# Kernel optimization log

Hardware: AMD Instinct MI355X
Metric: run time of the kernel (lower is better)

## Reference

```python
import jax, jax.numpy as jnp
import numpy as np

N_NODES = 10000
N_EDGES = 320000
HIDDEN = 256          # hidden_feat -> dim of gcn output x
MLP_IN = 2 * HIDDEN   # concat(src, dst)
OUT_FEATURES = 10


def setup_inputs() -> dict:
    key = jax.random.key(0)
    k_x, k_e, k_w1, k_w2 = jax.random.split(key, 4)
    x = jax.random.normal(k_x, (N_NODES, HIDDEN), dtype=jnp.float32)
    edge_index = jax.random.randint(k_e, (2, N_EDGES), 0, N_NODES, dtype=jnp.int64)
    # ClassifierMLP2(2*hidden_feat, out_features): Linear -> ReLU -> Linear -> log_softmax
    W1 = jax.random.normal(k_w1, (MLP_IN, HIDDEN), dtype=jnp.float32) * 0.02
    b1 = jnp.zeros((HIDDEN,), dtype=jnp.float32)
    W2 = jax.random.normal(k_w2, (HIDDEN, OUT_FEATURES), dtype=jnp.float32) * 0.02
    b2 = jnp.zeros((OUT_FEATURES,), dtype=jnp.float32)
    return {"x": x, "edge_index": edge_index, "W1": W1, "b1": b1, "W2": W2, "b2": b2}


def reference(x, edge_index, W1, b1, W2, b2):
    # mix_node_features(..., node_feat_mixing='cat'):
    # gather source/target node features per edge and concatenate -> [E, 2*H]
    src, dst = edge_index[0], edge_index[1]
    edges_x = jnp.concatenate([x[src], x[dst]], axis=1)  # [E, 2H]
    # ClassifierMLP2 forward
    h = jax.nn.relu(edges_x @ W1 + b1)                   # [E, H]
    logits = h @ W2 + b2                                 # [E, C]
    return jax.nn.log_softmax(logits, axis=-1)
```

## Files before the change

### kernel.cpp

```cpp
#include <hip/hip_runtime.h>

#define E_TOTAL 320000
#define NNODES  10000
#define HID     256
#define NCLS    10

typedef __attribute__((ext_vector_type(4))) float f32x4;
typedef __attribute__((ext_vector_type(2))) float f32x2;
typedef __attribute__((ext_vector_type(4))) unsigned int u32x4;
typedef __attribute__((ext_vector_type(8))) __bf16 bf16x8;
typedef __attribute__((ext_vector_type(8))) unsigned short u16x8;

static __device__ __forceinline__ unsigned short f2bf(float f) {
  unsigned u = __builtin_bit_cast(unsigned, f);
  u += 0x7fffu + ((u >> 16) & 1u);
  return (unsigned short)(u >> 16);
}

__global__ void k_pack(const float* __restrict__ x,
                       const float* __restrict__ W1,
                       const float* __restrict__ W2,
                       unsigned short* __restrict__ xbf,
                       unsigned short* __restrict__ w1f,
                       unsigned short* __restrict__ w2f) {
  int b = blockIdx.x, tid = threadIdx.x;
  if (b < 1250) {
    int i = b * 256 + tid;
    const f32x4* s = (const f32x4*)x + (size_t)i * 2;
    f32x4 a = s[0], c = s[1];
    u16x8 o;
    o[0]=f2bf(a[0]); o[1]=f2bf(a[1]); o[2]=f2bf(a[2]); o[3]=f2bf(a[3]);
    o[4]=f2bf(c[0]); o[5]=f2bf(c[1]); o[6]=f2bf(c[2]); o[7]=f2bf(c[3]);
    *((u16x8*)xbf + i) = o;
  } else if (b < 1314) {
    int gid = (b - 1250) * 256 + tid;
    int l = gid & 63, kk = (gid >> 6) & 7, cb = (gid >> 9) & 15, half = gid >> 13;
    int kbase = half * 256 + kk * 32 + (l >> 4) * 8;
    int col = cb * 16 + (l & 15);
    u16x8 o;
#pragma unroll
    for (int j = 0; j < 8; ++j) o[j] = f2bf(W1[(size_t)(kbase + j) * HID + col]);
    *((u16x8*)w1f + gid) = o;
  } else {
    int gid = (b - 1314) * 256 + tid;
    int l = gid & 63, kk = gid >> 6;
    int kbase = kk * 32 + (l >> 4) * 8;
    int c = l & 15;
    u16x8 o;
#pragma unroll
    for (int j = 0; j < 8; ++j)
      o[j] = (c < NCLS) ? f2bf(W2[(size_t)(kbase + j) * NCLS + c]) : (unsigned short)0;
    *((u16x8*)w2f + gid) = o;
  }
}

__global__ __launch_bounds__(256, 3) void k_prep(
    const unsigned short* __restrict__ xbf,
    const unsigned short* __restrict__ w1f,
    const float* __restrict__ b1,
    unsigned char* __restrict__ Yf8)
{
  __shared__ __align__(16) unsigned short ldsA[2][32 * 64];

  const int tid  = threadIdx.x;
  const int lane = tid & 63;
  const int wv   = tid >> 6;
  const int n0   = blockIdx.x * 32;
  const int half = blockIdx.y;
  const int l15  = lane & 15;
  const int lhi  = lane >> 4;

  f32x4 acc[2][4] = {};

  auto stageA = [&](int kb, int buf) {
    int col0 = kb * 64;
    int r = wv * 8 + (lane >> 3);
    int gr = n0 + r; if (gr > NNODES - 1) gr = NNODES - 1;
    int usrc = (lane & 7) ^ (r & 7);
    const unsigned short* g = xbf + (size_t)gr * HID + col0 + usrc * 8;
    unsigned short* lp = &ldsA[buf][(wv * 8) * 64];
    __builtin_amdgcn_global_load_lds(
        (const __attribute__((address_space(1))) unsigned int*)g,
        (__attribute__((address_space(3))) unsigned int*)lp,
        16, 0, 0);
  };

  stageA(0, 0);

  for (int kb = 0; kb < 4; ++kb) {
    int buf = kb & 1;
    __syncthreads();
    if (kb < 3) stageA(kb + 1, buf ^ 1);

    bf16x8 bfr[2][4];
#pragma unroll
    for (int ks = 0; ks < 2; ++ks)
#pragma unroll
      for (int n = 0; n < 4; ++n) {
        int cb = wv * 4 + n;
        int kk = kb * 2 + ks;
        int f = (half * 16 + cb) * 8 + kk;
        bfr[ks][n] = *(const bf16x8*)(w1f + ((size_t)f * 64 + lane) * 8);
      }

#pragma unroll
    for (int ks = 0; ks < 2; ++ks) {
      bf16x8 afr[2];
#pragma unroll
      for (int m = 0; m < 2; ++m) {
        int row = m * 16 + l15;
        int boff = row * 128 + ((ks * 64 + lhi * 16) ^ ((row & 7) << 4));
        afr[m] = *(const bf16x8*)((const char*)&ldsA[buf][0] + boff);
      }
#pragma unroll
      for (int m = 0; m < 2; ++m)
#pragma unroll
        for (int n = 0; n < 4; ++n)
          acc[m][n] = __builtin_amdgcn_mfma_f32_16x16x32_bf16(afr[m], bfr[ks][n], acc[m][n], 0, 0, 0);
    }
  }

  float b1v[4];
#pragma unroll
  for (int n = 0; n < 4; ++n) b1v[n] = (half == 0) ? b1[wv * 64 + n * 16 + l15] : 0.f;

#pragma unroll
  for (int m = 0; m < 2; ++m)
#pragma unroll
    for (int n = 0; n < 4; ++n) {
      int col = wv * 64 + n * 16 + l15;
      int pos = ((col >> 3) & 3) * 64 + ((col >> 5) << 3) + (col & 7);
#pragma unroll
      for (int r = 0; r < 4; ++r) {
        int row = m * 16 + lhi * 4 + r;
        int gr = n0 + row;
        if (gr < NNODES) {
          float v = acc[m][n][r] + b1v[n];
          int pk = __builtin_amdgcn_cvt_pk_fp8_f32(v, v, 0, false);
          Yf8[(size_t)gr * 512 + half * 256 + pos] = (unsigned char)(pk & 0xff);
        }
      }
    }
}

__global__ __launch_bounds__(256, 4) void k_edge(
    const int* __restrict__ ei,
    const unsigned char* __restrict__ Yf8,
    const unsigned short* __restrict__ w2f,
    const float* __restrict__ b2,
    float* __restrict__ out)
{
  __shared__ __align__(16) unsigned short ldsW[4096];

  const int tid  = threadIdx.x;
  const int lane = tid & 63;
  const int wv   = tid >> 6;
  const int e0   = blockIdx.x * 64;
  const int l15  = lane & 15;
  const int lhi  = lane >> 4;

  int edge = e0 + wv * 16 + l15;
  int src = ei[edge];
  int dst = ei[E_TOTAL + edge];

  {
    const u16x8* s = (const u16x8*)w2f;
    u16x8* d = (u16x8*)ldsW;
    d[tid] = s[tid];
    d[tid + 256] = s[tid + 256];
  }
  __syncthreads();

  const u32x4* q1 = (const u32x4*)(Yf8 + (size_t)src * 512 + lhi * 64);
  const u32x4* q2 = (const u32x4*)(Yf8 + (size_t)dst * 512 + 256 + lhi * 64);
  u32x4 ya[4], yb[4];
#pragma unroll
  for (int i = 0; i < 4; ++i) { ya[i] = q1[i]; yb[i] = q2[i]; }

  f32x4 lg = {0.f, 0.f, 0.f, 0.f};
#pragma unroll
  for (int kk = 0; kk < 8; ++kk) {
    bf16x8 bw = *(const bf16x8*)(ldsW + kk * 512 + lane * 8);
    unsigned a0 = ya[kk >> 1][(kk & 1) * 2], a1 = ya[kk >> 1][(kk & 1) * 2 + 1];
    unsigned c0 = yb[kk >> 1][(kk & 1) * 2], c1 = yb[kk >> 1][(kk & 1) * 2 + 1];
    f32x2 A0 = __builtin_amdgcn_cvt_pk_f32_fp8(a0, false);
    f32x2 A1 = __builtin_amdgcn_cvt_pk_f32_fp8(a0, true);
    f32x2 A2 = __builtin_amdgcn_cvt_pk_f32_fp8(a1, false);
    f32x2 A3 = __builtin_amdgcn_cvt_pk_f32_fp8(a1, true);
    f32x2 B0 = __builtin_amdgcn_cvt_pk_f32_fp8(c0, false);
    f32x2 B1 = __builtin_amdgcn_cvt_pk_f32_fp8(c0, true);
    f32x2 B2 = __builtin_amdgcn_cvt_pk_f32_fp8(c1, false);
    f32x2 B3 = __builtin_amdgcn_cvt_pk_f32_fp8(c1, true);
    bf16x8 hh;
    hh[0] = (__bf16)fmaxf(A0[0] + B0[0], 0.f);
    hh[1] = (__bf16)fmaxf(A0[1] + B0[1], 0.f);
    hh[2] = (__bf16)fmaxf(A1[0] + B1[0], 0.f);
    hh[3] = (__bf16)fmaxf(A1[1] + B1[1], 0.f);
    hh[4] = (__bf16)fmaxf(A2[0] + B2[0], 0.f);
    hh[5] = (__bf16)fmaxf(A2[1] + B2[1], 0.f);
    hh[6] = (__bf16)fmaxf(A3[0] + B3[0], 0.f);
    hh[7] = (__bf16)fmaxf(A3[1] + B3[1], 0.f);
    lg = __builtin_amdgcn_mfma_f32_16x16x32_bf16(hh, bw, lg, 0, 0, 0);
  }

  bool valid = (l15 < NCLS);
  float bias = valid ? b2[l15] : 0.f;
#pragma unroll
  for (int r = 0; r < 4; ++r) {
    float v = lg[r] + bias;
    float mv = valid ? v : -1e30f;
#pragma unroll
    for (int s = 1; s < 16; s <<= 1) mv = fmaxf(mv, __shfl_xor(mv, s, 64));
    float ev = valid ? __expf(v - mv) : 0.f;
    float sv = ev;
#pragma unroll
    for (int s = 1; s < 16; s <<= 1) sv += __shfl_xor(sv, s, 64);
    float res = v - mv - __logf(sv);
    if (valid) out[(size_t)(e0 + wv * 16 + lhi * 4 + r) * NCLS + l15] = res;
  }
}

extern "C" void kernel_launch(void* const* d_in, const int* in_sizes, int n_in,
                              void* d_out, int out_size, void* d_ws, size_t ws_size,
                              hipStream_t stream) {
  const float* x  = (const float*)d_in[0];
  const int*   ei = (const int*)d_in[1];
  const float* W1 = (const float*)d_in[2];
  const float* b1 = (const float*)d_in[3];
  const float* W2 = (const float*)d_in[4];
  const float* b2 = (const float*)d_in[5];
  float* out = (float*)d_out;

  unsigned short* xbf = (unsigned short*)d_ws;
  unsigned short* w1f = xbf + (size_t)NNODES * HID;
  unsigned short* w2f = w1f + (size_t)131072;
  unsigned char*  Yf8 = (unsigned char*)(w2f + 4096);

  k_pack<<<1316, 256, 0, stream>>>(x, W1, W2, xbf, w1f, w2f);
  k_prep<<<dim3((NNODES + 31) / 32, 2), 256, 0, stream>>>(xbf, w1f, b1, Yf8);
  k_edge<<<E_TOTAL / 64, 256, 0, stream>>>(ei, Yf8, w2f, b2, out);
}
```

Baseline: 52.75 us.

## Fuse x bf16 conversion into prep GEMM and merge both halves per block

Drops the separate pass that converts x to bf16 into a workspace buffer. The prep kernel now stages fp32 x rows into LDS with global_load_lds and converts to bf16 while building MFMA fragments. Each block also computes both W1 halves (512 output columns) in one launch instead of a 2D grid, so each x tile is loaded once. The cost is a larger accumulator set (16 f32x4 per wave), twice the LDS footprint and more conversion instructions in the inner loop, which may lower occupancy.

```diff
diff --git a/kernel.cpp b/kernel.cpp
--- a/kernel.cpp
+++ b/kernel.cpp
@@ -17,23 +17,13 @@
   return (unsigned short)(u >> 16);
 }
 
-__global__ void k_pack(const float* __restrict__ x,
-                       const float* __restrict__ W1,
+__global__ void k_pack(const float* __restrict__ W1,
                        const float* __restrict__ W2,
-                       unsigned short* __restrict__ xbf,
                        unsigned short* __restrict__ w1f,
                        unsigned short* __restrict__ w2f) {
   int b = blockIdx.x, tid = threadIdx.x;
-  if (b < 1250) {
-    int i = b * 256 + tid;
-    const f32x4* s = (const f32x4*)x + (size_t)i * 2;
-    f32x4 a = s[0], c = s[1];
-    u16x8 o;
-    o[0]=f2bf(a[0]); o[1]=f2bf(a[1]); o[2]=f2bf(a[2]); o[3]=f2bf(a[3]);
-    o[4]=f2bf(c[0]); o[5]=f2bf(c[1]); o[6]=f2bf(c[2]); o[7]=f2bf(c[3]);
-    *((u16x8*)xbf + i) = o;
-  } else if (b < 1314) {
-    int gid = (b - 1250) * 256 + tid;
+  if (b < 64) {
+    int gid = b * 256 + tid;
     int l = gid & 63, kk = (gid >> 6) & 7, cb = (gid >> 9) & 15, half = gid >> 13;
     int kbase = half * 256 + kk * 32 + (l >> 4) * 8;
     int col = cb * 16 + (l & 15);
@@ -42,7 +32,7 @@
     for (int j = 0; j < 8; ++j) o[j] = f2bf(W1[(size_t)(kbase + j) * HID + col]);
     *((u16x8*)w1f + gid) = o;
   } else {
-    int gid = (b - 1314) * 256 + tid;
+    int gid = (b - 64) * 256 + tid;
     int l = gid & 63, kk = gid >> 6;
     int kbase = kk * 32 + (l >> 4) * 8;
     int c = l & 15;
@@ -55,53 +45,45 @@
 }
 
 __global__ __launch_bounds__(256, 3) void k_prep(
-    const unsigned short* __restrict__ xbf,
+    const float* __restrict__ x,
     const unsigned short* __restrict__ w1f,
     const float* __restrict__ b1,
     unsigned char* __restrict__ Yf8)
 {
-  __shared__ __align__(16) unsigned short ldsA[2][32 * 64];
+  __shared__ __align__(16) float ldsX[2][32 * 64];
 
   const int tid  = threadIdx.x;
   const int lane = tid & 63;
   const int wv   = tid >> 6;
   const int n0   = blockIdx.x * 32;
-  const int half = blockIdx.y;
   const int l15  = lane & 15;
   const int lhi  = lane >> 4;
-
-  f32x4 acc[2][4] = {};
-
-  auto stageA = [&](int kb, int buf) {
-    int col0 = kb * 64;
-    int r = wv * 8 + (lane >> 3);
-    int gr = n0 + r; if (gr > NNODES - 1) gr = NNODES - 1;
-    int usrc = (lane & 7) ^ (r & 7);
-    const unsigned short* g = xbf + (size_t)gr * HID + col0 + usrc * 8;
-    unsigned short* lp = &ldsA[buf][(wv * 8) * 64];
-    __builtin_amdgcn_global_load_lds(
-        (const __attribute__((address_space(1))) unsigned int*)g,
-        (__attribute__((address_space(3))) unsigned int*)lp,
-        16, 0, 0);
+  const int half = wv >> 1;
+
+  f32x4 acc[2][8] = {};
+
+  auto stageX = [&](int kb, int buf) {
+#pragma unroll
+    for (int i = 0; i < 2; ++i) {
+      int row = i * 16 + wv * 4 + (lane >> 4);
+      int gr = n0 + row; if (gr > NNODES - 1) gr = NNODES - 1;
+      int c = lane & 15;
+      int csrc = ((((c >> 1) ^ (row & 7)) << 1) | (c & 1));
+      const float* g = x + (size_t)gr * HID + kb * 64 + csrc * 4;
+      float* lp = &ldsX[buf][(i * 16 + wv * 4) * 64];
+      __builtin_amdgcn_global_load_lds(
+          (const __attribute__((address_space(1))) unsigned int*)g,
+          (__attribute__((address_space(3))) unsigned int*)lp,
+          16, 0, 0);
+    }
   };
 
-  stageA(0, 0);
+  stageX(0, 0);
 
   for (int kb = 0; kb < 4; ++kb) {
     int buf = kb & 1;
     __syncthreads();
-    if (kb < 3) stageA(kb + 1, buf ^ 1);
-
-    bf16x8 bfr[2][4];
-#pragma unroll
-    for (int ks = 0; ks < 2; ++ks)
-#pragma unroll
-      for (int n = 0; n < 4; ++n) {
-        int cb = wv * 4 + n;
-        int kk = kb * 2 + ks;
-        int f = (half * 16 + cb) * 8 + kk;
-        bfr[ks][n] = *(const bf16x8*)(w1f + ((size_t)f * 64 + lane) * 8);
-      }
+    if (kb < 3) stageX(kb + 1, buf ^ 1);
 
 #pragma unroll
     for (int ks = 0; ks < 2; ++ks) {
@@ -109,27 +91,42 @@
 #pragma unroll
       for (int m = 0; m < 2; ++m) {
         int row = m * 16 + l15;
-        int boff = row * 128 + ((ks * 64 + lhi * 16) ^ ((row & 7) << 4));
-        afr[m] = *(const bf16x8*)((const char*)&ldsA[buf][0] + boff);
+        int u = (ks * 4 + lhi) ^ (row & 7);
+        const float* p = &ldsX[buf][0] + row * 64 + u * 8;
+        f32x4 lo = *(const f32x4*)p;
+        f32x4 hi = *(const f32x4*)(p + 4);
+        bf16x8 t;
+        t[0] = (__bf16)lo[0]; t[1] = (__bf16)lo[1];
+        t[2] = (__bf16)lo[2]; t[3] = (__bf16)lo[3];
+        t[4] = (__bf16)hi[0]; t[5] = (__bf16)hi[1];
+        t[6] = (__bf16)hi[2]; t[7] = (__bf16)hi[3];
+        afr[m] = t;
       }
-#pragma unroll
-      for (int m = 0; m < 2; ++m)
-#pragma unroll
-        for (int n = 0; n < 4; ++n)
-          acc[m][n] = __builtin_amdgcn_mfma_f32_16x16x32_bf16(afr[m], bfr[ks][n], acc[m][n], 0, 0, 0);
+      int kk = kb * 2 + ks;
+#pragma unroll
+      for (int n = 0; n < 8; ++n) {
+        int cb = (wv & 1) * 8 + n;
+        int f = (half * 16 + cb) * 8 + kk;
+        bf16x8 bfr = *(const bf16x8*)(w1f + ((size_t)f * 64 + lane) * 8);
+#pragma unroll
+        for (int m = 0; m < 2; ++m)
+          acc[m][n] = __builtin_amdgcn_mfma_f32_16x16x32_bf16(afr[m], bfr, acc[m][n], 0, 0, 0);
+      }
     }
   }
 
-  float b1v[4];
-#pragma unroll
-  for (int n = 0; n < 4; ++n) b1v[n] = (half == 0) ? b1[wv * 64 + n * 16 + l15] : 0.f;
+  float b1v[8];
+#pragma unroll
+  for (int n = 0; n < 8; ++n)
+    b1v[n] = (half == 0) ? b1[(wv & 1) * 128 + n * 16 + l15] : 0.f;
 
 #pragma unroll
   for (int m = 0; m < 2; ++m)
 #pragma unroll
-    for (int n = 0; n < 4; ++n) {
-      int col = wv * 64 + n * 16 + l15;
-      int pos = ((col >> 3) & 3) * 64 + ((col >> 5) << 3) + (col & 7);
+    for (int n = 0; n < 8; ++n) {
+      int colg = wv * 128 + n * 16 + l15;
+      int c = colg & 255;
+      int pos = ((c >> 3) & 3) * 64 + ((c >> 5) << 3) + (c & 7);
 #pragma unroll
       for (int r = 0; r < 4; ++r) {
         int row = m * 16 + lhi * 4 + r;
@@ -231,12 +228,12 @@
   const float* b2 = (const float*)d_in[5];
   float* out = (float*)d_out;
 
-  unsigned short* xbf = (unsigned short*)d_ws;
-  unsigned short* w1f = xbf + (size_t)NNODES * HID;
-  unsigned short* w2f = w1f + (size_t)131072;
-  unsigned char*  Yf8 = (unsigned char*)(w2f + 4096);
-
-  k_pack<<<1316, 256, 0, stream>>>(x, W1, W2, xbf, w1f, w2f);
-  k_prep<<<dim3((NNODES + 31) / 32, 2), 256, 0, stream>>>(xbf, w1f, b1, Yf8);
+  char* ws = (char*)d_ws;
+  unsigned short* w1f = (unsigned short*)ws;
+  unsigned short* w2f = (unsigned short*)(ws + 262144);
+  unsigned char*  Yf8 = (unsigned char*)(ws + 270336);
+
+  k_pack<<<66, 256, 0, stream>>>(W1, W2, w1f, w2f);
+  k_prep<<<(NNODES + 31) / 32, 256, 0, stream>>>(x, w1f, b1, Yf8);
   k_edge<<<E_TOTAL / 64, 256, 0, stream>>>(ei, Yf8, w2f, b2, out);
 }
```

Measured after the change: 68.92 us. 30.7% more time.
